# Kernel optimization log

Measured on AMD Instinct MI355X. Metric: run time of the kernel, lower is better.

The kernel has to match this reference:

```python
import jax, jax.numpy as jnp
import numpy as np

IN_DIM = 256
NUM_HEADS = 8
HEAD_DIM = IN_DIM // NUM_HEADS


def setup_inputs() -> dict:
    key = jax.random.key(0)
    k1, k2, k3, k4, k5, k6 = jax.random.split(key, 6)
    B, C, H, W = 2, IN_DIM, 64, 64
    scale = 1.0 / np.sqrt(IN_DIM)
    return {
        "tgt": jax.random.normal(k1, (B, C, H, W), dtype=jnp.float32),
        "src": jax.random.normal(k2, (B, C, H, W), dtype=jnp.float32),
        # nn.Linear weights stored as [out, in] (torch convention); y = x @ W.T
        "Wq": jax.random.normal(k3, (IN_DIM, IN_DIM), dtype=jnp.float32) * scale,
        "Wk": jax.random.normal(k4, (IN_DIM, IN_DIM), dtype=jnp.float32) * scale,
        "Wv": jax.random.normal(k5, (IN_DIM, IN_DIM), dtype=jnp.float32) * scale,
        "Wo": jax.random.normal(k6, (IN_DIM, IN_DIM), dtype=jnp.float32) * scale,
    }


def reference(tgt, src, Wq, Wk, Wv, Wo):
    B, C, H, W = src.shape
    N = H * W
    # b c h w -> b (h w) c
    src_t = src.reshape(B, C, N).transpose(0, 2, 1)
    tgt_t = tgt.reshape(B, C, N).transpose(0, 2, 1)
    # project and split heads: [B, N, C] -> [B, heads, N, head_dim]
    def heads(x, Wt):
        y = jnp.einsum('bnc,dc->bnd', x, Wt)
        return y.reshape(B, N, NUM_HEADS, HEAD_DIM).transpose(0, 2, 1, 3)
    q = heads(tgt_t, Wq)
    k = heads(src_t, Wk)
    v = heads(src_t, Wv)
    scores = jnp.einsum('bhqd,bhkd->bhqk', q, k) / jnp.sqrt(jnp.float32(HEAD_DIM))
    attn = jax.nn.softmax(scores, axis=-1)
    weighted = jnp.einsum('bhqk,bhkd->bhqd', attn, v)  # [B, heads, N, head_dim]
    weighted = weighted.transpose(0, 2, 1, 3).reshape(B, N, C)
    out = jnp.einsum('bnc,dc->bnd', weighted + tgt_t, Wo)
    return out
```

## Files before the change

kernel.cpp:

```cpp
#include <hip/hip_runtime.h>
#include <hip/hip_bf16.h>

#define IN_DIM 256
#define NHEADS 8
#define HDIM 32
#define BATCH 2
#define NTOK 4096
#define QSCALE (0.17677669529663687f * 1.4426950408889634f)

typedef __hip_bfloat16 bf16;
typedef __attribute__((ext_vector_type(8))) short bf16x8;
typedef __attribute__((ext_vector_type(4))) short bf16x4;
typedef __attribute__((ext_vector_type(4))) float f32x4;

union bfrag { bf16x8 v; bf16x4 h[2]; };

__device__ __forceinline__ float b2f(bf16 x) { return __bfloat162float(x); }

#if __has_builtin(__builtin_amdgcn_exp2f)
__device__ __forceinline__ float fast_exp2(float x) { return __builtin_amdgcn_exp2f(x); }
#else
__device__ __forceinline__ float fast_exp2(float x) { return exp2f(x); }
#endif

__device__ __forceinline__ unsigned packbf2(float a, float b) {
    union { __hip_bfloat162 h; unsigned u; } c;
    c.h = __float22bfloat162_rn(float2{a, b});
    return c.u;
}

#if __has_builtin(__builtin_amdgcn_mfma_f32_16x16x16bf16_1k)
__device__ __forceinline__ f32x4 mfma16(bf16x4 a, bf16x4 b, f32x4 c) {
    return __builtin_amdgcn_mfma_f32_16x16x16bf16_1k(a, b, c, 0, 0, 0);
}
#else
__device__ __forceinline__ f32x4 mfma16(bf16x4 a, bf16x4 b, f32x4 c) {
    bf16x8 az = {a[0], a[1], a[2], a[3], 0, 0, 0, 0};
    bf16x8 bz = {b[0], b[1], b[2], b[3], 0, 0, 0, 0};
    return __builtin_amdgcn_mfma_f32_16x16x32_bf16(az, bz, c, 0, 0, 0);
}
#endif

__device__ __forceinline__ void pack16(float4 a, float4 b, float4 c, float4 d,
                                       bf16* dst) {
    uint2 w0 = {packbf2(a.x, a.y), packbf2(a.z, a.w)};
    uint2 w1 = {packbf2(b.x, b.y), packbf2(b.z, b.w)};
    uint2 w2 = {packbf2(c.x, c.y), packbf2(c.z, c.w)};
    uint2 w3 = {packbf2(d.x, d.y), packbf2(d.z, d.w)};
    *(uint2*)(dst + 0)  = w0;
    *(uint2*)(dst + 4)  = w1;
    *(uint2*)(dst + 8)  = w2;
    *(uint2*)(dst + 12) = w3;
}

__global__ __launch_bounds__(256) void proj_mfma(
    const float* __restrict__ tgt, const float* __restrict__ src,
    const float* __restrict__ Wq, const float* __restrict__ Wk,
    const float* __restrict__ Wv,
    bf16* __restrict__ Qo, bf16* __restrict__ Ko, bf16* __restrict__ Vo)
{
    const int which = blockIdx.y;
    const int dh = blockIdx.z;
    const int b  = blockIdx.x >> 7;
    const int n0 = (blockIdx.x & 127) * 32;
    const float* X = (which == 0) ? tgt : src;
    const float* W = (which == 0) ? Wq : (which == 1 ? Wk : Wv);

    const int tid = threadIdx.x;
    const int wave = tid >> 6, lane = tid & 63;
    const int lg = lane >> 4, lc = lane & 15;
    const int wn = wave & 1, wdq = wave >> 1;

    __shared__ bf16 As[32 * 260];
    __shared__ bf16 Ws[2][128 * 36];

    {
        const float* Xb = X + (size_t)b * IN_DIM * NTOK + n0;
        for (int it = 0; it < 8; ++it) {
            int idx = it * 256 + tid;
            int c = idx >> 3, j4 = idx & 7;
            float4 x = *(const float4*)(Xb + (size_t)c * NTOK + j4 * 4);
            As[(j4 * 4 + 0) * 260 + c] = __float2bfloat16(x.x);
            As[(j4 * 4 + 1) * 260 + c] = __float2bfloat16(x.y);
            As[(j4 * 4 + 2) * 260 + c] = __float2bfloat16(x.z);
            As[(j4 * 4 + 3) * 260 + c] = __float2bfloat16(x.w);
        }
    }
    const int wd = tid >> 1, wc = (tid & 1) * 16;
    const float* Wbase = W + (size_t)(dh * 128 + wd) * IN_DIM + wc;
    {
        float4 a = *(const float4*)(Wbase + 0);
        float4 bb = *(const float4*)(Wbase + 4);
        float4 cc = *(const float4*)(Wbase + 8);
        float4 dd = *(const float4*)(Wbase + 12);
        pack16(a, bb, cc, dd, &Ws[0][wd * 36 + wc]);
    }
    __syncthreads();

    f32x4 acc[4];
    #pragma unroll
    for (int t = 0; t < 4; ++t) acc[t] = f32x4{0.f, 0.f, 0.f, 0.f};

    for (int s = 0; s < 8; ++s) {
        const int c0 = s * 32;
        float4 pa, pb, pc, pd;
        if (s < 7) {
            const float* wn_ = Wbase + (s + 1) * 32;
            pa = *(const float4*)(wn_ + 0);
            pb = *(const float4*)(wn_ + 4);
            pc = *(const float4*)(wn_ + 8);
            pd = *(const float4*)(wn_ + 12);
        }
        bfrag af;
        const bf16* ap = &As[(wn * 16 + lc) * 260 + c0 + lg * 8];
        af.h[0] = *(const bf16x4*)ap;
        af.h[1] = *(const bf16x4*)(ap + 4);
        #pragma unroll
        for (int t = 0; t < 4; ++t) {
            bfrag wf;
            const bf16* wp = &Ws[s & 1][(wdq * 64 + t * 16 + lc) * 36 + lg * 8];
            wf.h[0] = *(const bf16x4*)wp;
            wf.h[1] = *(const bf16x4*)(wp + 4);
            acc[t] = __builtin_amdgcn_mfma_f32_16x16x32_bf16(af.v, wf.v, acc[t], 0, 0, 0);
        }
        if (s < 7) {
            __syncthreads();
            pack16(pa, pb, pc, pd, &Ws[(s + 1) & 1][wd * 36 + wc]);
            __syncthreads();
        }
    }

    const int nb = n0 + wn * 16 + lg * 4;
    if (which == 2) {
        #pragma unroll
        for (int t = 0; t < 4; ++t) {
            int d = dh * 128 + wdq * 64 + t * 16 + lc;
            uint2 pk;
            pk.x = packbf2(acc[t][0], acc[t][1]);
            pk.y = packbf2(acc[t][2], acc[t][3]);
            *(uint2*)(Vo + ((size_t)b * IN_DIM + d) * NTOK + nb) = pk;
        }
    } else {
        const float sc = (which == 0) ? QSCALE : 1.0f;
        bf16* O = (which == 0) ? Qo : Ko;
        #pragma unroll
        for (int t = 0; t < 4; ++t)
            #pragma unroll
            for (int r = 0; r < 4; ++r)
                O[((size_t)b * NTOK + nb + r) * IN_DIM + dh * 128 + wdq * 64 + t * 16 + lc]
                    = __float2bfloat16(acc[t][r] * sc);
    }
}

__global__ __launch_bounds__(256) void attn_mfma_kernel(
    const bf16* __restrict__ Q, const bf16* __restrict__ K,
    const bf16* __restrict__ Vt, const float* __restrict__ tgt,
    bf16* __restrict__ Wt)
{
    const int blk = blockIdx.x;
    const int bh  = 2 * (blk & 7) + ((blk >> 3) & 1);
    const int qb  = blk >> 4;
    const int b = bh >> 3, h = bh & 7;
    const int tid  = threadIdx.x;
    const int wave = tid >> 6;
    const int lane = tid & 63;
    const int lg = lane >> 4, lc = lane & 15;
    const int qw = qb * 64 + wave * 16;

    __shared__ bf16 KL[2][64 * 40];
    __shared__ bf16 VL[2][32 * 72];

    const bf16x8 qf = *(const bf16x8*)(Q + ((size_t)b * NTOK + qw + lc) * IN_DIM
                                         + h * HDIM + lg * 8);

    bf16x4 ones4;
    #pragma unroll
    for (int i = 0; i < 4; ++i) ((short*)&ones4)[i] = (short)0x3F80;
    const f32x4 z = {0.f, 0.f, 0.f, 0.f};

    const int srow = tid >> 2, sd = (tid & 3) * 8;
    const int vrow = tid >> 3, vch = tid & 7;
    const int kwoff = srow * 40 + sd;
    const int vwoff = vrow * 72 + vch * 8;
    const int kroff = lc * 40 + lg * 8;
    const int vroff0 = lc * 72 + lg * 4;
    const int vroff1 = (16 + lc) * 72 + lg * 4;

    const bf16* Kp = K  + ((size_t)b * NTOK + srow) * IN_DIM + h * HDIM + sd;
    const bf16* Vp = Vt + ((size_t)b * IN_DIM + h * HDIM + vrow) * NTOK + vch * 8;

    f32x4 o0 = {0.f,0.f,0.f,0.f}, o1 = {0.f,0.f,0.f,0.f}, ol = {0.f,0.f,0.f,0.f};

    bf16x8 kreg = *(const bf16x8*)Kp;
    bf16x8 vreg = *(const bf16x8*)Vp;
    Kp += (size_t)64 * IN_DIM;
    Vp += 64;

#define HALF(CUR)                                                              \
    {                                                                          \
        *(bf16x8*)&KL[CUR][kwoff] = kreg;                                      \
        *(bf16x8*)&VL[CUR][vwoff] = vreg;                                      \
        kreg = *(const bf16x8*)Kp;                                             \
        vreg = *(const bf16x8*)Vp;                                             \
        Kp += (size_t)64 * IN_DIM;                                             \
        Vp += 64;                                                              \
        __syncthreads();                                                       \
        f32x4 s[4];                                                            \
        _Pragma("unroll")                                                      \
        for (int t = 0; t < 4; ++t) {                                          \
            bf16x8 kf = *(const bf16x8*)&KL[CUR][kroff + t * 640];             \
            s[t] = __builtin_amdgcn_mfma_f32_16x16x32_bf16(kf, qf, z, 0,0,0);  \
        }                                                                      \
        _Pragma("unroll")                                                      \
        for (int t = 0; t < 4; ++t) {                                          \
            bf16x4 v0 = *(const bf16x4*)&VL[CUR][vroff0 + t * 16];             \
            bf16x4 v1 = *(const bf16x4*)&VL[CUR][vroff1 + t * 16];             \
            union { bf16x4 h; uint2 u; } pk;                                   \
            pk.u.x = packbf2(fast_exp2(s[t][0]), fast_exp2(s[t][1]));          \
            pk.u.y = packbf2(fast_exp2(s[t][2]), fast_exp2(s[t][3]));          \
            o0 = mfma16(pk.h, v0, o0);                                         \
            o1 = mfma16(pk.h, v1, o1);                                         \
            ol = mfma16(pk.h, ones4, ol);                                      \
        }                                                                      \
    }

    for (int it = 0; it < NTOK / 128; ++it) {
        HALF(0)
        HALF(1)
    }
#undef HALF

    const float* tg0 = tgt + ((size_t)b * IN_DIM + h * HDIM + lc) * NTOK + qw + lg * 4;
    float4 r0 = *(const float4*)tg0;
    float4 r1 = *(const float4*)(tg0 + (size_t)16 * NTOK);

    bf16* op = Wt + ((size_t)b * NTOK + qw + lg * 4) * IN_DIM + h * HDIM + lc;
    #pragma unroll
    for (int r = 0; r < 4; ++r) {
        float inv = 1.f / ol[r];
        op[(size_t)r * IN_DIM]      = __float2bfloat16(o0[r] * inv + (&r0.x)[r]);
        op[(size_t)r * IN_DIM + 16] = __float2bfloat16(o1[r] * inv + (&r1.x)[r]);
    }
}

__global__ __launch_bounds__(256) void out_mfma(
    const bf16* __restrict__ A, const float* __restrict__ Wo,
    float* __restrict__ out)
{
    const int dh = blockIdx.y;
    const int b  = blockIdx.x >> 7;
    const int n0 = (blockIdx.x & 127) * 32;

    const int tid = threadIdx.x;
    const int wave = tid >> 6, lane = tid & 63;
    const int lg = lane >> 4, lc = lane & 15;
    const int wn = wave & 1, wdq = wave >> 1;

    __shared__ bf16 As[32 * 260];
    __shared__ bf16 Ws[2][128 * 36];

    {
        const bf16* Ab = A + ((size_t)b * NTOK + n0) * IN_DIM;
        for (int it = 0; it < 4; ++it) {
            int idx = it * 256 + tid;
            int r = idx >> 5, ch = idx & 31;
            bfrag v;
            v.v = *(const bf16x8*)(Ab + (size_t)r * IN_DIM + ch * 8);
            *(bf16x4*)&As[r * 260 + ch * 8]     = v.h[0];
            *(bf16x4*)&As[r * 260 + ch * 8 + 4] = v.h[1];
        }
    }
    const int wd = tid >> 1, wc = (tid & 1) * 16;
    const float* Wbase = Wo + (size_t)(dh * 128 + wd) * IN_DIM + wc;
    {
        float4 a = *(const float4*)(Wbase + 0);
        float4 bb = *(const float4*)(Wbase + 4);
        float4 cc = *(const float4*)(Wbase + 8);
        float4 dd = *(const float4*)(Wbase + 12);
        pack16(a, bb, cc, dd, &Ws[0][wd * 36 + wc]);
    }
    __syncthreads();

    f32x4 acc[4];
    #pragma unroll
    for (int t = 0; t < 4; ++t) acc[t] = f32x4{0.f, 0.f, 0.f, 0.f};

    for (int s = 0; s < 8; ++s) {
        const int c0 = s * 32;
        float4 pa, pb, pc, pd;
        if (s < 7) {
            const float* wn_ = Wbase + (s + 1) * 32;
            pa = *(const float4*)(wn_ + 0);
            pb = *(const float4*)(wn_ + 4);
            pc = *(const float4*)(wn_ + 8);
            pd = *(const float4*)(wn_ + 12);
        }
        bfrag af;
        const bf16* ap = &As[(wn * 16 + lc) * 260 + c0 + lg * 8];
        af.h[0] = *(const bf16x4*)ap;
        af.h[1] = *(const bf16x4*)(ap + 4);
        #pragma unroll
        for (int t = 0; t < 4; ++t) {
            bfrag wf;
            const bf16* wp = &Ws[s & 1][(wdq * 64 + t * 16 + lc) * 36 + lg * 8];
            wf.h[0] = *(const bf16x4*)wp;
            wf.h[1] = *(const bf16x4*)(wp + 4);
            acc[t] = __builtin_amdgcn_mfma_f32_16x16x32_bf16(af.v, wf.v, acc[t], 0, 0, 0);
        }
        if (s < 7) {
            __syncthreads();
            pack16(pa, pb, pc, pd, &Ws[(s + 1) & 1][wd * 36 + wc]);
            __syncthreads();
        }
    }

    const int nb = n0 + wn * 16 + lg * 4;
    #pragma unroll
    for (int t = 0; t < 4; ++t)
        #pragma unroll
        for (int r = 0; r < 4; ++r)
            out[((size_t)b * NTOK + nb + r) * IN_DIM + dh * 128 + wdq * 64 + t * 16 + lc]
                = acc[t][r];
}

extern "C" void kernel_launch(void* const* d_in, const int* in_sizes, int n_in,
                              void* d_out, int out_size, void* d_ws, size_t ws_size,
                              hipStream_t stream) {
    const float* tgt = (const float*)d_in[0];
    const float* src = (const float*)d_in[1];
    const float* Wq  = (const float*)d_in[2];
    const float* Wk  = (const float*)d_in[3];
    const float* Wv  = (const float*)d_in[4];
    const float* Wo  = (const float*)d_in[5];
    float* out = (float*)d_out;

    const size_t SZ = (size_t)BATCH * NTOK * IN_DIM * sizeof(bf16);
    char* w = (char*)d_ws;
    bf16* Qb  = (bf16*)(w);
    bf16* Kb  = (bf16*)(w + SZ);
    bf16* Vtb = (bf16*)(w + 2 * SZ);
    bf16* Wt  = (bf16*)(w + 3 * SZ);

    proj_mfma<<<dim3(256, 3, 2), 256, 0, stream>>>(tgt, src, Wq, Wk, Wv, Qb, Kb, Vtb);

    attn_mfma_kernel<<<1024, 256, 0, stream>>>(Qb, Kb, Vtb, tgt, Wt);

    out_mfma<<<dim3(256, 2), 256, 0, stream>>>(Wt, Wo, out);
}
```

Measured before the change: 102.3 us.

## Process two query tiles per wave in attention to reuse K/V fragments

Each wave now handles 32 queries (two 16-row MFMA tiles) instead of 16, so every K/V fragment loaded from LDS feeds twice as many MFMAs and half as many blocks stream K/V from global memory. The grid is halved to 512 blocks. s_setprio hints are placed around the MFMA groups so that matrix work interleaves with the exp2 and pack work of other waves. In exchange, register pressure rises and there are fewer blocks to cover the 256 CUs.

```diff
diff --git a/kernel.cpp b/kernel.cpp
--- a/kernel.cpp
+++ b/kernel.cpp
@@ -165,13 +165,15 @@
     const int wave = tid >> 6;
     const int lane = tid & 63;
     const int lg = lane >> 4, lc = lane & 15;
-    const int qw = qb * 64 + wave * 16;
+    const int qw = qb * 128 + wave * 32;
 
     __shared__ bf16 KL[2][64 * 40];
     __shared__ bf16 VL[2][32 * 72];
 
-    const bf16x8 qf = *(const bf16x8*)(Q + ((size_t)b * NTOK + qw + lc) * IN_DIM
-                                         + h * HDIM + lg * 8);
+    const bf16x8 qfa = *(const bf16x8*)(Q + ((size_t)b * NTOK + qw + lc) * IN_DIM
+                                          + h * HDIM + lg * 8);
+    const bf16x8 qfb = *(const bf16x8*)(Q + ((size_t)b * NTOK + qw + 16 + lc) * IN_DIM
+                                          + h * HDIM + lg * 8);
 
     bf16x4 ones4;
     #pragma unroll
@@ -189,7 +191,8 @@
     const bf16* Kp = K  + ((size_t)b * NTOK + srow) * IN_DIM + h * HDIM + sd;
     const bf16* Vp = Vt + ((size_t)b * IN_DIM + h * HDIM + vrow) * NTOK + vch * 8;
 
-    f32x4 o0 = {0.f,0.f,0.f,0.f}, o1 = {0.f,0.f,0.f,0.f}, ol = {0.f,0.f,0.f,0.f};
+    f32x4 o0a = {0.f,0.f,0.f,0.f}, o1a = {0.f,0.f,0.f,0.f}, ola = {0.f,0.f,0.f,0.f};
+    f32x4 o0b = {0.f,0.f,0.f,0.f}, o1b = {0.f,0.f,0.f,0.f}, olb = {0.f,0.f,0.f,0.f};
 
     bf16x8 kreg = *(const bf16x8*)Kp;
     bf16x8 vreg = *(const bf16x8*)Vp;
@@ -205,22 +208,39 @@
         Kp += (size_t)64 * IN_DIM;                                             \
         Vp += 64;                                                              \
         __syncthreads();                                                       \
-        f32x4 s[4];                                                            \
+        bf16x8 kf[4];                                                          \
+        _Pragma("unroll")                                                      \
+        for (int t = 0; t < 4; ++t)                                            \
+            kf[t] = *(const bf16x8*)&KL[CUR][kroff + t * 640];                 \
+        bf16x4 v0[4], v1[4];                                                   \
         _Pragma("unroll")                                                      \
         for (int t = 0; t < 4; ++t) {                                          \
-            bf16x8 kf = *(const bf16x8*)&KL[CUR][kroff + t * 640];             \
-            s[t] = __builtin_amdgcn_mfma_f32_16x16x32_bf16(kf, qf, z, 0,0,0);  \
+            v0[t] = *(const bf16x4*)&VL[CUR][vroff0 + t * 16];                 \
+            v1[t] = *(const bf16x4*)&VL[CUR][vroff1 + t * 16];                 \
         }                                                                      \
+        f32x4 sa[4], sb[4];                                                    \
+        __builtin_amdgcn_s_setprio(1);                                         \
         _Pragma("unroll")                                                      \
         for (int t = 0; t < 4; ++t) {                                          \
-            bf16x4 v0 = *(const bf16x4*)&VL[CUR][vroff0 + t * 16];             \
-            bf16x4 v1 = *(const bf16x4*)&VL[CUR][vroff1 + t * 16];             \
-            union { bf16x4 h; uint2 u; } pk;                                   \
-            pk.u.x = packbf2(fast_exp2(s[t][0]), fast_exp2(s[t][1]));          \
-            pk.u.y = packbf2(fast_exp2(s[t][2]), fast_exp2(s[t][3]));          \
-            o0 = mfma16(pk.h, v0, o0);                                         \
-            o1 = mfma16(pk.h, v1, o1);                                         \
-            ol = mfma16(pk.h, ones4, ol);                                      \
+            sa[t] = __builtin_amdgcn_mfma_f32_16x16x32_bf16(kf[t], qfa, z, 0,0,0); \
+            sb[t] = __builtin_amdgcn_mfma_f32_16x16x32_bf16(kf[t], qfb, z, 0,0,0); \
+        }                                                                      \
+        __builtin_amdgcn_s_setprio(0);                                         \
+        _Pragma("unroll")                                                      \
+        for (int t = 0; t < 4; ++t) {                                          \
+            union { bf16x4 h; uint2 u; } pka, pkb;                             \
+            pka.u.x = packbf2(fast_exp2(sa[t][0]), fast_exp2(sa[t][1]));       \
+            pka.u.y = packbf2(fast_exp2(sa[t][2]), fast_exp2(sa[t][3]));       \
+            pkb.u.x = packbf2(fast_exp2(sb[t][0]), fast_exp2(sb[t][1]));       \
+            pkb.u.y = packbf2(fast_exp2(sb[t][2]), fast_exp2(sb[t][3]));       \
+            __builtin_amdgcn_s_setprio(1);                                     \
+            o0a = mfma16(pka.h, v0[t], o0a);                                   \
+            o1a = mfma16(pka.h, v1[t], o1a);                                   \
+            ola = mfma16(pka.h, ones4, ola);                                   \
+            o0b = mfma16(pkb.h, v0[t], o0b);                                   \
+            o1b = mfma16(pkb.h, v1[t], o1b);                                   \
+            olb = mfma16(pkb.h, ones4, olb);                                   \
+            __builtin_amdgcn_s_setprio(0);                                     \
         }                                                                      \
     }
 
@@ -230,16 +250,22 @@
     }
 #undef HALF
 
-    const float* tg0 = tgt + ((size_t)b * IN_DIM + h * HDIM + lc) * NTOK + qw + lg * 4;
-    float4 r0 = *(const float4*)tg0;
-    float4 r1 = *(const float4*)(tg0 + (size_t)16 * NTOK);
-
-    bf16* op = Wt + ((size_t)b * NTOK + qw + lg * 4) * IN_DIM + h * HDIM + lc;
+    const float* tga = tgt + ((size_t)b * IN_DIM + h * HDIM + lc) * NTOK + qw + lg * 4;
+    float4 r0a = *(const float4*)tga;
+    float4 r1a = *(const float4*)(tga + (size_t)16 * NTOK);
+    float4 r0b = *(const float4*)(tga + 16);
+    float4 r1b = *(const float4*)(tga + (size_t)16 * NTOK + 16);
+
+    bf16* opa = Wt + ((size_t)b * NTOK + qw + lg * 4) * IN_DIM + h * HDIM + lc;
+    bf16* opb = opa + (size_t)16 * IN_DIM;
     #pragma unroll
     for (int r = 0; r < 4; ++r) {
-        float inv = 1.f / ol[r];
-        op[(size_t)r * IN_DIM]      = __float2bfloat16(o0[r] * inv + (&r0.x)[r]);
-        op[(size_t)r * IN_DIM + 16] = __float2bfloat16(o1[r] * inv + (&r1.x)[r]);
+        float inva = 1.f / ola[r];
+        float invb = 1.f / olb[r];
+        opa[(size_t)r * IN_DIM]      = __float2bfloat16(o0a[r] * inva + (&r0a.x)[r]);
+        opa[(size_t)r * IN_DIM + 16] = __float2bfloat16(o1a[r] * inva + (&r1a.x)[r]);
+        opb[(size_t)r * IN_DIM]      = __float2bfloat16(o0b[r] * invb + (&r0b.x)[r]);
+        opb[(size_t)r * IN_DIM + 16] = __float2bfloat16(o1b[r] * invb + (&r1b.x)[r]);
     }
 }
 
@@ -343,7 +369,7 @@
 
     proj_mfma<<<dim3(256, 3, 2), 256, 0, stream>>>(tgt, src, Wq, Wk, Wv, Qb, Kb, Vtb);
 
-    attn_mfma_kernel<<<1024, 256, 0, stream>>>(Qb, Kb, Vtb, tgt, Wt);
+    attn_mfma_kernel<<<512, 256, 0, stream>>>(Qb, Kb, Vtb, tgt, Wt);
 
     out_mfma<<<dim3(256, 2), 256, 0, stream>>>(Wt, Wo, out);
 }
```

Result: no change. 100.9 us (-1.4%).

## Split attention KV range across two wave groups and use 16x16x32 PV MFMAs

Applied to the files above, without the earlier changes.

The attention kernel now launches 512 threads per block. Two groups of four waves each process half of the key/value sequence with their own double-buffered LDS tiles, and the partial accumulators are reduced through shared memory at the end. The P·V and row-sum products switch from paired 16x16x16 MFMAs to single 16x16x32 MFMAs over two key tiles, with LDS loads hoisted ahead and s_setprio around the MFMA bursts. This is meant to add parallelism per query block and halve MFMA issue count, at the cost of more LDS, a larger block and an extra reduction step.

```diff
diff --git a/kernel.cpp b/kernel.cpp
--- a/kernel.cpp
+++ b/kernel.cpp
@@ -28,18 +28,6 @@
     c.h = __float22bfloat162_rn(float2{a, b});
     return c.u;
 }
-
-#if __has_builtin(__builtin_amdgcn_mfma_f32_16x16x16bf16_1k)
-__device__ __forceinline__ f32x4 mfma16(bf16x4 a, bf16x4 b, f32x4 c) {
-    return __builtin_amdgcn_mfma_f32_16x16x16bf16_1k(a, b, c, 0, 0, 0);
-}
-#else
-__device__ __forceinline__ f32x4 mfma16(bf16x4 a, bf16x4 b, f32x4 c) {
-    bf16x8 az = {a[0], a[1], a[2], a[3], 0, 0, 0, 0};
-    bf16x8 bz = {b[0], b[1], b[2], b[3], 0, 0, 0, 0};
-    return __builtin_amdgcn_mfma_f32_16x16x32_bf16(az, bz, c, 0, 0, 0);
-}
-#endif
 
 __device__ __forceinline__ void pack16(float4 a, float4 b, float4 c, float4 d,
                                        bf16* dst) {
@@ -152,7 +140,9 @@
     }
 }
 
-__global__ __launch_bounds__(256) void attn_mfma_kernel(
+#define KLSZ (64 * 40)
+#define VLSZ (32 * 72)
+__global__ __launch_bounds__(512) void attn_mfma_kernel(
     const bf16* __restrict__ Q, const bf16* __restrict__ K,
     const bf16* __restrict__ Vt, const float* __restrict__ tgt,
     bf16* __restrict__ Wt)
@@ -163,31 +153,36 @@
     const int b = bh >> 3, h = bh & 7;
     const int tid  = threadIdx.x;
     const int wave = tid >> 6;
+    const int grp  = wave >> 2;
+    const int wl   = wave & 3;
     const int lane = tid & 63;
     const int lg = lane >> 4, lc = lane & 15;
-    const int qw = qb * 64 + wave * 16;
-
-    __shared__ bf16 KL[2][64 * 40];
-    __shared__ bf16 VL[2][32 * 72];
+    const int qw = qb * 64 + wl * 16;
+
+    __shared__ __align__(16) char pool[(2 * 2 * (KLSZ + VLSZ)) * 2];
+    bf16* KL = (bf16*)pool;
+    bf16* VL = (bf16*)(pool + 2 * 2 * KLSZ * 2);
+    float* redC = (float*)pool;
 
     const bf16x8 qf = *(const bf16x8*)(Q + ((size_t)b * NTOK + qw + lc) * IN_DIM
                                          + h * HDIM + lg * 8);
 
-    bf16x4 ones4;
+    bf16x8 ones8;
     #pragma unroll
-    for (int i = 0; i < 4; ++i) ((short*)&ones4)[i] = (short)0x3F80;
+    for (int i = 0; i < 8; ++i) ((short*)&ones8)[i] = (short)0x3F80;
     const f32x4 z = {0.f, 0.f, 0.f, 0.f};
 
-    const int srow = tid >> 2, sd = (tid & 3) * 8;
-    const int vrow = tid >> 3, vch = tid & 7;
-    const int kwoff = srow * 40 + sd;
-    const int vwoff = vrow * 72 + vch * 8;
-    const int kroff = lc * 40 + lg * 8;
-    const int vroff0 = lc * 72 + lg * 4;
-    const int vroff1 = (16 + lc) * 72 + lg * 4;
-
-    const bf16* Kp = K  + ((size_t)b * NTOK + srow) * IN_DIM + h * HDIM + sd;
-    const bf16* Vp = Vt + ((size_t)b * IN_DIM + h * HDIM + vrow) * NTOK + vch * 8;
+    const int tg   = tid & 255;
+    const int srow = tg >> 2, sd = (tg & 3) * 8;
+    const int vrow = tg >> 3, vch = tg & 7;
+    const int kwoff = grp * 2 * KLSZ + srow * 40 + sd;
+    const int vwoff = grp * 2 * VLSZ + vrow * 72 + vch * 8;
+    const int kroff = grp * 2 * KLSZ + lc * 40 + lg * 8;
+    const int vroff0 = grp * 2 * VLSZ + lc * 72 + lg * 4;
+    const int vroff1 = grp * 2 * VLSZ + (16 + lc) * 72 + lg * 4;
+
+    const bf16* Kp = K  + ((size_t)b * NTOK + grp * 2048 + srow) * IN_DIM + h * HDIM + sd;
+    const bf16* Vp = Vt + ((size_t)b * IN_DIM + h * HDIM + vrow) * NTOK + grp * 2048 + vch * 8;
 
     f32x4 o0 = {0.f,0.f,0.f,0.f}, o1 = {0.f,0.f,0.f,0.f}, ol = {0.f,0.f,0.f,0.f};
 
@@ -198,50 +193,80 @@
 
 #define HALF(CUR)                                                              \
     {                                                                          \
-        *(bf16x8*)&KL[CUR][kwoff] = kreg;                                      \
-        *(bf16x8*)&VL[CUR][vwoff] = vreg;                                      \
+        *(bf16x8*)&KL[kwoff + (CUR) * KLSZ] = kreg;                            \
+        *(bf16x8*)&VL[vwoff + (CUR) * VLSZ] = vreg;                            \
         kreg = *(const bf16x8*)Kp;                                             \
         vreg = *(const bf16x8*)Vp;                                             \
         Kp += (size_t)64 * IN_DIM;                                             \
         Vp += 64;                                                              \
         __syncthreads();                                                       \
-        f32x4 s[4];                                                            \
+        bf16x8 kf[4];                                                          \
+        _Pragma("unroll")                                                      \
+        for (int t = 0; t < 4; ++t)                                            \
+            kf[t] = *(const bf16x8*)&KL[kroff + (CUR) * KLSZ + t * 640];       \
+        bf16x4 v0[4], v1[4];                                                   \
         _Pragma("unroll")                                                      \
         for (int t = 0; t < 4; ++t) {                                          \
-            bf16x8 kf = *(const bf16x8*)&KL[CUR][kroff + t * 640];             \
-            s[t] = __builtin_amdgcn_mfma_f32_16x16x32_bf16(kf, qf, z, 0,0,0);  \
+            v0[t] = *(const bf16x4*)&VL[vroff0 + (CUR) * VLSZ + t * 16];       \
+            v1[t] = *(const bf16x4*)&VL[vroff1 + (CUR) * VLSZ + t * 16];       \
         }                                                                      \
+        f32x4 s[4];                                                            \
+        __builtin_amdgcn_s_setprio(1);                                         \
         _Pragma("unroll")                                                      \
-        for (int t = 0; t < 4; ++t) {                                          \
-            bf16x4 v0 = *(const bf16x4*)&VL[CUR][vroff0 + t * 16];             \
-            bf16x4 v1 = *(const bf16x4*)&VL[CUR][vroff1 + t * 16];             \
-            union { bf16x4 h; uint2 u; } pk;                                   \
-            pk.u.x = packbf2(fast_exp2(s[t][0]), fast_exp2(s[t][1]));          \
-            pk.u.y = packbf2(fast_exp2(s[t][2]), fast_exp2(s[t][3]));          \
-            o0 = mfma16(pk.h, v0, o0);                                         \
-            o1 = mfma16(pk.h, v1, o1);                                         \
-            ol = mfma16(pk.h, ones4, ol);                                      \
+        for (int t = 0; t < 4; ++t)                                            \
+            s[t] = __builtin_amdgcn_mfma_f32_16x16x32_bf16(kf[t], qf, z, 0,0,0); \
+        __builtin_amdgcn_s_setprio(0);                                         \
+        _Pragma("unroll")                                                      \
+        for (int tcp = 0; tcp < 2; ++tcp) {                                    \
+            union { bf16x8 v; uint4 u; } pa;                                   \
+            pa.u.x = packbf2(fast_exp2(s[2*tcp][0]),   fast_exp2(s[2*tcp][1]));   \
+            pa.u.y = packbf2(fast_exp2(s[2*tcp][2]),   fast_exp2(s[2*tcp][3]));   \
+            pa.u.z = packbf2(fast_exp2(s[2*tcp+1][0]), fast_exp2(s[2*tcp+1][1])); \
+            pa.u.w = packbf2(fast_exp2(s[2*tcp+1][2]), fast_exp2(s[2*tcp+1][3])); \
+            bfrag B0, B1;                                                      \
+            B0.h[0] = v0[2*tcp]; B0.h[1] = v0[2*tcp+1];                        \
+            B1.h[0] = v1[2*tcp]; B1.h[1] = v1[2*tcp+1];                        \
+            __builtin_amdgcn_s_setprio(1);                                     \
+            o0 = __builtin_amdgcn_mfma_f32_16x16x32_bf16(pa.v, B0.v, o0, 0,0,0); \
+            o1 = __builtin_amdgcn_mfma_f32_16x16x32_bf16(pa.v, B1.v, o1, 0,0,0); \
+            ol = __builtin_amdgcn_mfma_f32_16x16x32_bf16(pa.v, ones8, ol, 0,0,0); \
+            __builtin_amdgcn_s_setprio(0);                                     \
         }                                                                      \
     }
 
-    for (int it = 0; it < NTOK / 128; ++it) {
+    for (int it = 0; it < NTOK / 256; ++it) {
         HALF(0)
         HALF(1)
     }
 #undef HALF
 
-    const float* tg0 = tgt + ((size_t)b * IN_DIM + h * HDIM + lc) * NTOK + qw + lg * 4;
-    float4 r0 = *(const float4*)tg0;
-    float4 r1 = *(const float4*)(tg0 + (size_t)16 * NTOK);
-
-    bf16* op = Wt + ((size_t)b * NTOK + qw + lg * 4) * IN_DIM + h * HDIM + lc;
-    #pragma unroll
-    for (int r = 0; r < 4; ++r) {
-        float inv = 1.f / ol[r];
-        op[(size_t)r * IN_DIM]      = __float2bfloat16(o0[r] * inv + (&r0.x)[r]);
-        op[(size_t)r * IN_DIM + 16] = __float2bfloat16(o1[r] * inv + (&r1.x)[r]);
-    }
-}
+    __syncthreads();
+    if (grp) {
+        float* d = &redC[(wl * 64 + lane) * 12];
+        *(f32x4*)(d + 0) = o0;  *(f32x4*)(d + 4) = o1;  *(f32x4*)(d + 8) = ol;
+    }
+    __syncthreads();
+    if (!grp) {
+        const float* s = &redC[(wl * 64 + lane) * 12];
+        o0 += *(const f32x4*)(s + 0);
+        o1 += *(const f32x4*)(s + 4);
+        ol += *(const f32x4*)(s + 8);
+
+        const float* tg0 = tgt + ((size_t)b * IN_DIM + h * HDIM + lc) * NTOK + qw + lg * 4;
+        float4 r0 = *(const float4*)tg0;
+        float4 r1 = *(const float4*)(tg0 + (size_t)16 * NTOK);
+
+        bf16* op = Wt + ((size_t)b * NTOK + qw + lg * 4) * IN_DIM + h * HDIM + lc;
+        #pragma unroll
+        for (int r = 0; r < 4; ++r) {
+            float inv = 1.f / ol[r];
+            op[(size_t)r * IN_DIM]      = __float2bfloat16(o0[r] * inv + (&r0.x)[r]);
+            op[(size_t)r * IN_DIM + 16] = __float2bfloat16(o1[r] * inv + (&r1.x)[r]);
+        }
+    }
+}
+#undef KLSZ
+#undef VLSZ
 
 __global__ __launch_bounds__(256) void out_mfma(
     const bf16* __restrict__ A, const float* __restrict__ Wo,
@@ -343,7 +368,7 @@
 
     proj_mfma<<<dim3(256, 3, 2), 256, 0, stream>>>(tgt, src, Wq, Wk, Wv, Qb, Kb, Vtb);
 
-    attn_mfma_kernel<<<1024, 256, 0, stream>>>(Qb, Kb, Vtb, tgt, Wt);
+    attn_mfma_kernel<<<1024, 512, 0, stream>>>(Qb, Kb, Vtb, tgt, Wt);
 
     out_mfma<<<dim3(256, 2), 256, 0, stream>>>(Wt, Wo, out);
 }
```

Measured after the change: 96.43 us. -5.7%, faster.
